# Kernel tuning notes

Hardware: AMD Instinct MI355X
Metric: run time of the kernel (lower is better)

Reference implementation:

```python
import jax, jax.numpy as jnp
import numpy as np
import math

S, HID = 2048, 2048
NH, Q_LORA, KV_LORA = 16, 1536, 512
NOPE, ROPE, VDIM = 128, 64, 128
HEAD = NOPE + ROPE  # 192
BLK = 128
EPS = 1e-6
MSCALE = 0.1 * 1.0 * math.log(40.0) + 1.0
SOFTMAX_SCALE = HEAD ** -0.5 * MSCALE * MSCALE


def _dequant(w, s, blk=BLK):
    # w: [out,in] stored quantized values, s: [ceil(out/blk), ceil(in/blk)] block scale_inv
    so = jnp.repeat(s, blk, axis=0)[: w.shape[0]]
    se = jnp.repeat(so, blk, axis=1)[:, : w.shape[1]]
    return w * se


def _mm_dq(x, w, s):
    # mm_w8a16_dq_forward: x @ dequant(w).T
    return x @ _dequant(w, s).T


def _rmsnorm(x, w, eps=EPS):
    var = jnp.mean(x * x, axis=-1, keepdims=True)
    return x * jax.lax.rsqrt(var + eps) * w


def _rotate_half(x):
    h = x.shape[-1] // 2
    return jnp.concatenate([-x[..., h:], x[..., :h]], axis=-1)


def setup_inputs() -> dict:
    key = jax.random.key(0)
    ks = jax.random.split(key, 16)
    d = {
        'hidden_states': jax.random.normal(ks[0], (S, HID), jnp.float32),
        'wq_a': jax.random.normal(ks[1], (Q_LORA, HID), jnp.float32),
        'sq_a': jax.random.uniform(ks[2], (12, 16), jnp.float32) * 0.02 + 0.005,
        'wq_b': jax.random.normal(ks[3], (NH * HEAD, Q_LORA), jnp.float32),
        'sq_b': jax.random.uniform(ks[4], (24, 12), jnp.float32) * 0.02 + 0.005,
        'wkv_a': jax.random.normal(ks[5], (KV_LORA + ROPE, HID), jnp.float32),
        'skv_a': jax.random.uniform(ks[6], (5, 16), jnp.float32) * 0.02 + 0.005,
        'wkv_b': jax.random.normal(ks[7], (NH * (NOPE + VDIM), KV_LORA), jnp.float32),
        'skv_b': jax.random.uniform(ks[8], (32, 4), jnp.float32) * 0.02 + 0.005,
        'wo': jax.random.normal(ks[9], (HID, NH * VDIM), jnp.float32),
        'so': jax.random.uniform(ks[10], (16, 16), jnp.float32) * 0.02 + 0.005,
        'q_ln_w': jnp.ones((Q_LORA,), jnp.float32),
        'kv_ln_w': jnp.ones((KV_LORA,), jnp.float32),
    }
    pos = jnp.arange(S, dtype=jnp.float32)[:, None]
    inv = 1.0 / (10000.0 ** (jnp.arange(0, ROPE, 2, dtype=jnp.float32) / ROPE))
    ang = pos * inv[None, :]
    ang = jnp.concatenate([ang, ang], axis=-1)  # [S, 64]
    d['cos'] = jnp.cos(ang)
    d['sin'] = jnp.sin(ang)
    return d


def reference(hidden_states, cos, sin, wq_a, sq_a, wq_b, sq_b, wkv_a, skv_a,
              wkv_b, skv_b, wo, so, q_ln_w, kv_ln_w):
    # Q low-rank path: q_a -> rmsnorm -> q_b
    lq = _mm_dq(hidden_states, wq_a, sq_a)                 # [S, q_lora]
    q = _mm_dq(_rmsnorm(lq, q_ln_w), wq_b, sq_b)           # [S, NH*HEAD]
    q = q.reshape(S, NH, HEAD)
    q_nope, q_pe = q[..., :NOPE], q[..., NOPE:]            # [S,NH,128], [S,NH,64]

    # KV low-rank + MQA rope path
    lkv = _mm_dq(hidden_states, wkv_a, skv_a)              # [S, kv_lora+rope]
    kv_nope = _rmsnorm(lkv[:, :KV_LORA], kv_ln_w)          # [S, kv_lora]
    k_pe = lkv[:, KV_LORA:]                                # [S, 64] (shared across heads)
    kvb = _mm_dq(kv_nope, wkv_b, skv_b).reshape(S, NH, NOPE + VDIM)
    k_nope, v = kvb[..., :NOPE], kvb[..., NOPE:]           # [S,NH,128] each

    # RoPE (rotate-half) on the pe parts
    q_pe = q_pe * cos[:, None, :] + _rotate_half(q_pe) * sin[:, None, :]
    k_pe = k_pe * cos + _rotate_half(k_pe) * sin           # [S, 64]

    # prefill MLA attention with causal mask
    scores = (jnp.einsum('shd,thd->hst', q_nope, k_nope)
              + jnp.einsum('shd,td->hst', q_pe, k_pe)) * SOFTMAX_SCALE
    causal = jnp.tril(jnp.ones((S, S), bool))
    scores = jnp.where(causal[None], scores, -jnp.inf)
    probs = jax.nn.softmax(scores, axis=-1)                # [NH,S,S]
    attn = jnp.einsum('hst,thd->shd', probs, v).reshape(S, NH * VDIM)

    return _mm_dq(attn, wo, so)                            # [S, HID]
```

## Files before the change

### kernel.cpp

```cpp
#include <hip/hip_runtime.h>
#include <hip/hip_bf16.h>

typedef unsigned short u16;
typedef unsigned int u32;
typedef __attribute__((ext_vector_type(8))) short bf16x8;
typedef __attribute__((ext_vector_type(4))) float f32x4;
typedef __attribute__((ext_vector_type(16))) float f32x16;
typedef __attribute__((ext_vector_type(4))) unsigned short u16x4;

#define S_LEN 2048
#define HIDDEN 2048
#define NHEAD 16
#define QLORA 1536
#define KVLORA 512
#define NOPE_D 128
#define ROPE_D 64
#define V_D 128
#define HEAD_D 192
#define NCOMB 2176
#define LOG2E 1.442695041f

__device__ __constant__ float SM_SCALE_C = (float)(0.07216878364870323 *
    ((0.1 * 3.6888794541139363 + 1.0) * (0.1 * 3.6888794541139363 + 1.0)));

__device__ inline u16 f2bf(float f) {
    __hip_bfloat16 h = __float2bfloat16(f);
    return *reinterpret_cast<u16*>(&h);
}
__device__ inline u32 pack2bf(float lo, float hi) {
    float2 v = make_float2(lo, hi);
    __hip_bfloat162 h2 = __float22bfloat162_rn(v);
    return *reinterpret_cast<u32*>(&h2);
}
__device__ inline float bf2f(u16 b) {
    union { unsigned int u; float f; } v; v.u = ((unsigned int)b) << 16;
    return v.f;
}
__device__ inline void gload_lds16(const u16* g, u16* l) {
    __builtin_amdgcn_global_load_lds(
        (const __attribute__((address_space(1))) void*)g,
        (__attribute__((address_space(3))) void*)l, 16, 0, 0);
}

__device__ __forceinline__ int xcd_swizzle(int orig, int nwg) {
    int qq = nwg >> 3, rr = nwg & 7, xcd = orig & 7, loc = orig >> 3;
    return (xcd < rr) ? (xcd * (qq + 1) + loc)
                      : (rr * (qq + 1) + (xcd - rr) * qq + loc);
}

__global__ __launch_bounds__(256)
void prep_weights(const float* __restrict__ hs,
                  const float* __restrict__ wq_a, const float* __restrict__ sq_a,
                  const float* __restrict__ wq_b, const float* __restrict__ sq_b,
                  const float* __restrict__ wkv_a, const float* __restrict__ skv_a,
                  const float* __restrict__ wkv_b, const float* __restrict__ skv_b,
                  const float* __restrict__ wo, const float* __restrict__ so,
                  u16* __restrict__ hs_bf, u16* __restrict__ wcomb,
                  u16* __restrict__ wqb_bf, u16* __restrict__ wkvb_bf,
                  u16* __restrict__ wo_bf) {
    int r = blockIdx.x * 4 + (threadIdx.x >> 6);
    const float* W; const float* Sc; u16* out; int n, K, sc_cols;
    if (r < 2048)       { W = hs;    Sc = 0;      out = hs_bf;   n = r;        K = 2048; sc_cols = 0; }
    else if (r < 3584)  { W = wq_a;  Sc = sq_a;   out = wcomb;   n = r - 2048; K = 2048; sc_cols = 16; }
    else if (r < 4160)  { W = wkv_a; Sc = skv_a;  out = wcomb + (size_t)QLORA * 2048; n = r - 3584; K = 2048; sc_cols = 16; }
    else if (r < 7232)  { W = wq_b;  Sc = sq_b;   out = wqb_bf;  n = r - 4160; K = 1536; sc_cols = 12; }
    else if (r < 11328) { W = wkv_b; Sc = skv_b;  out = wkvb_bf; n = r - 7232; K = 512;  sc_cols = 4; }
    else                { W = wo;    Sc = so;     out = wo_bf;   n = r - 11328; K = 2048; sc_cols = 16; }
    for (int k = (threadIdx.x & 63) * 8; k < K; k += 512) {
        float sc = Sc ? Sc[(n >> 7) * sc_cols + (k >> 7)] : 1.0f;
        f32x4 v0 = *(const f32x4*)(W + (size_t)n * K + k);
        f32x4 v1 = *(const f32x4*)(W + (size_t)n * K + k + 4);
        u32 w[4];
        w[0] = pack2bf(v0[0] * sc, v0[1] * sc);
        w[1] = pack2bf(v0[2] * sc, v0[3] * sc);
        w[2] = pack2bf(v1[0] * sc, v1[1] * sc);
        w[3] = pack2bf(v1[2] * sc, v1[3] * sc);
        *(__attribute__((ext_vector_type(4))) u32*)(out + (size_t)n * K + k) =
            *( __attribute__((ext_vector_type(4))) u32*)w;
    }
}

__device__ __forceinline__ void gemm_core(
    const u16* __restrict__ A, const u16* __restrict__ W, u16* __restrict__ C,
    int M, int N, int Ktot, int Ksub, int bm, int bn, int bz,
    u16 (*As)[128 * 64], u16 (*Ws)[128 * 64]) {
    const int tid = threadIdx.x;
    const int lane = tid & 63;
    const int wv = tid >> 6;
    const int wm = wv >> 1, wn = wv & 1;
    const int lr = lane & 15, lk = lane >> 4;
    const int srow = lane >> 3;
    const int schunk = lane & 7;

    f32x4 acc[4][4] = {};

    const int kbeg = bz * Ksub;
    const int nst = Ksub >> 6;

    auto stage = [&](int buf, int k0) {
        #pragma unroll
        for (int i = 0; i < 4; ++i) {
            int t = (wv * 4 + i) * 8 + srow;
            int cs = (schunk ^ (t & 7)) << 3;
            gload_lds16(A + (size_t)(bm + t) * Ktot + k0 + cs, &As[buf][(wv * 4 + i) * 512]);
            gload_lds16(W + (size_t)(bn + t) * Ktot + k0 + cs, &Ws[buf][(wv * 4 + i) * 512]);
        }
    };

    stage(0, kbeg);
    __syncthreads();
    int cur = 0;
    for (int t = 0; t < nst; ++t) {
        if (t + 1 < nst) stage(cur ^ 1, kbeg + (t + 1) * 64);
        #pragma unroll
        for (int kh = 0; kh < 2; ++kh) {
            bf16x8 af[4], bfr[4];
            #pragma unroll
            for (int mi = 0; mi < 4; ++mi) {
                int r = wm * 64 + mi * 16 + lr;
                af[mi] = *(const bf16x8*)&As[cur][r * 64 + (((kh * 4 + lk) ^ (lr & 7)) << 3)];
            }
            #pragma unroll
            for (int ni = 0; ni < 4; ++ni) {
                int r = wn * 64 + ni * 16 + lr;
                bfr[ni] = *(const bf16x8*)&Ws[cur][r * 64 + (((kh * 4 + lk) ^ (lr & 7)) << 3)];
            }
            __builtin_amdgcn_s_setprio(1);
            #pragma unroll
            for (int mi = 0; mi < 4; ++mi)
                #pragma unroll
                for (int ni = 0; ni < 4; ++ni)
                    acc[mi][ni] = __builtin_amdgcn_mfma_f32_16x16x32_bf16(af[mi], bfr[ni], acc[mi][ni], 0, 0, 0);
            __builtin_amdgcn_s_setprio(0);
        }
        __syncthreads();
        cur ^= 1;
    }

    u16* Pb = C + (size_t)bz * M * N;
    #pragma unroll
    for (int mi = 0; mi < 4; ++mi)
        #pragma unroll
        for (int ni = 0; ni < 4; ++ni)
            #pragma unroll
            for (int j = 0; j < 4; ++j) {
                int r = bm + wm * 64 + mi * 16 + lk * 4 + j;
                int c = bn + wn * 64 + ni * 16 + lr;
                if (c < N) Pb[(size_t)r * N + c] = f2bf(acc[mi][ni][j]);
            }
}

__global__ __launch_bounds__(256)
void gemm_bf16(const u16* __restrict__ A, const u16* __restrict__ W,
               u16* __restrict__ C, int M, int N, int Ktot, int Ksub) {
    __shared__ u16 As[2][128 * 64];
    __shared__ u16 Ws[2][128 * 64];
    const int gx = gridDim.x, gy = gridDim.y;
    const int nwg = gx * gy * gridDim.z;
    const int orig = blockIdx.x + gx * (blockIdx.y + gy * blockIdx.z);
    const int wg = xcd_swizzle(orig, nwg);
    const int bn = (wg % gx) * 128;
    const int bm = ((wg / gx) % gy) * 128;
    const int bz = wg / (gx * gy);
    gemm_core(A, W, C, M, N, Ktot, Ksub, bm, bn, bz, As, Ws);
}

__global__ __launch_bounds__(256)
void gemm_qh_kvb(const u16* __restrict__ lqn, const u16* __restrict__ wqb, u16* __restrict__ arena,
                 const u16* __restrict__ kvn, const u16* __restrict__ wkvb, u16* __restrict__ kvb) {
    __shared__ u16 As[2][128 * 64];
    __shared__ u16 Ws[2][128 * 64];
    const int NWG = 24 * 16 * 3 + 32 * 16;
    const int wg = xcd_swizzle(blockIdx.x, NWG);
    if (wg < 24 * 16 * 3) {
        const int bn = (wg % 24) * 128;
        const int bm = ((wg / 24) % 16) * 128;
        const int bz = wg / (24 * 16);
        gemm_core(lqn, wqb, arena, S_LEN, NHEAD * HEAD_D, QLORA, 512, bm, bn, bz, As, Ws);
    } else {
        const int w2 = wg - 24 * 16 * 3;
        const int bn = (w2 % 32) * 128;
        const int bm = (w2 / 32) * 128;
        gemm_core(kvn, wkvb, kvb, S_LEN, NHEAD * 256, KVLORA, 512, bm, bn, 0, As, Ws);
    }
}

__global__ __launch_bounds__(256)
void reduce_rms_comb(const u16* __restrict__ P,
                     const float* __restrict__ q_ln, const float* __restrict__ kv_ln,
                     u16* __restrict__ lqn, u16* __restrict__ kvn, u16* __restrict__ kpe) {
    __shared__ float vbuf[NCOMB];
    __shared__ float r2[2][4];
    const int row = blockIdx.x;
    const u16* p0 = P + (size_t)row * NCOMB;
    const size_t st = (size_t)S_LEN * NCOMB;
    float ssq = 0.f, ssk = 0.f;
    for (int c = threadIdx.x * 8; c < NCOMB; c += 2048) {
        bf16x8 a0 = *(const bf16x8*)(p0 + c);
        bf16x8 a1 = *(const bf16x8*)(p0 + st + c);
        bf16x8 a2 = *(const bf16x8*)(p0 + 2 * st + c);
        bf16x8 a3 = *(const bf16x8*)(p0 + 3 * st + c);
        float s = 0.f;
        #pragma unroll
        for (int j = 0; j < 8; ++j) {
            float v = bf2f((u16)a0[j]) + bf2f((u16)a1[j]) + bf2f((u16)a2[j]) + bf2f((u16)a3[j]);
            vbuf[c + j] = v;
            s += v * v;
        }
        if (c < QLORA) ssq += s;
        else if (c < QLORA + KVLORA) ssk += s;
    }
    #pragma unroll
    for (int off = 1; off < 64; off <<= 1) {
        ssq += __shfl_xor(ssq, off, 64);
        ssk += __shfl_xor(ssk, off, 64);
    }
    if ((threadIdx.x & 63) == 0) {
        r2[0][threadIdx.x >> 6] = ssq;
        r2[1][threadIdx.x >> 6] = ssk;
    }
    __syncthreads();
    float rsq = rsqrtf((r2[0][0] + r2[0][1] + r2[0][2] + r2[0][3]) / (float)QLORA + 1e-6f);
    float rsk = rsqrtf((r2[1][0] + r2[1][1] + r2[1][2] + r2[1][3]) / (float)KVLORA + 1e-6f);
    for (int c = threadIdx.x * 8; c < NCOMB; c += 2048) {
        bf16x8 o;
        if (c < QLORA) {
            #pragma unroll
            for (int j = 0; j < 8; ++j) o[j] = (short)f2bf(vbuf[c + j] * rsq * q_ln[c + j]);
            *(bf16x8*)(lqn + (size_t)row * QLORA + c) = o;
        } else if (c < QLORA + KVLORA) {
            int cc = c - QLORA;
            #pragma unroll
            for (int j = 0; j < 8; ++j) o[j] = (short)f2bf(vbuf[c + j] * rsk * kv_ln[cc + j]);
            *(bf16x8*)(kvn + (size_t)row * KVLORA + cc) = o;
        } else if (c < QLORA + KVLORA + ROPE_D) {
            int cc = c - QLORA - KVLORA;
            #pragma unroll
            for (int j = 0; j < 8; ++j) o[j] = (short)f2bf(vbuf[c + j]);
            *(bf16x8*)(kpe + (size_t)row * ROPE_D + cc) = o;
        }
    }
}

__global__ __launch_bounds__(256)
void prep_qkv_frag(const u16* __restrict__ P, const u16* __restrict__ kvb,
                   const u16* __restrict__ kpe, const float* __restrict__ cosb,
                   const float* __restrict__ sinb, u16* __restrict__ qfrag,
                   u16* __restrict__ kfrag, u16* __restrict__ vfrag) {
    __shared__ u16 Vs[32][136];
    const int sblk = blockIdx.x, h = blockIdx.y;
    if (blockIdx.z == 0) {
        const float sm = SM_SCALE_C;
        const size_t st = (size_t)S_LEN * (NHEAD * HEAD_D);
        #pragma unroll
        for (int c = 0; c < 3; ++c) {
            int idx = c * 256 + threadIdx.x;
            int kk = idx >> 6;
            int lane = idx & 63;
            int s = sblk * 32 + (lane & 31);
            int d0 = kk * 16 + (lane >> 5) * 8;
            const u16* p0 = P + (size_t)s * (NHEAD * HEAD_D) + h * HEAD_D;
            float x[8];
            {
                bf16x8 a0 = *(const bf16x8*)(p0 + d0);
                bf16x8 a1 = *(const bf16x8*)(p0 + st + d0);
                bf16x8 a2 = *(const bf16x8*)(p0 + 2 * st + d0);
                #pragma unroll
                for (int j = 0; j < 8; ++j)
                    x[j] = bf2f((u16)a0[j]) + bf2f((u16)a1[j]) + bf2f((u16)a2[j]);
            }
            bf16x8 o;
            if (d0 < NOPE_D) {
                #pragma unroll
                for (int j = 0; j < 8; ++j) o[j] = (short)f2bf(x[j] * sm);
            } else {
                int r0 = d0 - NOPE_D;
                int rp = (r0 + 32) & 63;
                float rv[8];
                bf16x8 b0 = *(const bf16x8*)(p0 + NOPE_D + rp);
                bf16x8 b1 = *(const bf16x8*)(p0 + st + NOPE_D + rp);
                bf16x8 b2 = *(const bf16x8*)(p0 + 2 * st + NOPE_D + rp);
                #pragma unroll
                for (int j = 0; j < 8; ++j)
                    rv[j] = bf2f((u16)b0[j]) + bf2f((u16)b1[j]) + bf2f((u16)b2[j]);
                float sign = (r0 < 32) ? -1.f : 1.f;
                #pragma unroll
                for (int j = 0; j < 8; ++j) {
                    float cs = cosb[s * ROPE_D + r0 + j];
                    float sn = sinb[s * ROPE_D + r0 + j];
                    o[j] = (short)f2bf((x[j] * cs + sign * rv[j] * sn) * sm);
                }
            }
            *(bf16x8*)(qfrag + (((size_t)h * 64 + sblk) * 12 + kk) * 512 + lane * 8) = o;
        }
    } else {
        #pragma unroll
        for (int it = 0; it < 2; ++it) {
            int idx = it * 256 + threadIdx.x;
            int r = idx >> 4;
            int c8 = (idx & 15) * 8;
            int s = sblk * 32 + r;
            *(bf16x8*)&Vs[r][c8] = *(const bf16x8*)(kvb + (size_t)s * (NHEAD * 256) + h * 256 + NOPE_D + c8);
        }
        #pragma unroll
        for (int c = 0; c < 3; ++c) {
            int idx = c * 256 + threadIdx.x;
            int kk = idx >> 6;
            int lane = idx & 63;
            int s = sblk * 32 + (lane & 31);
            int d0 = kk * 16 + (lane >> 5) * 8;
            bf16x8 o;
            if (d0 < NOPE_D) {
                o = *(const bf16x8*)(kvb + (size_t)s * (NHEAD * 256) + h * 256 + d0);
            } else {
                int r0 = d0 - NOPE_D;
                const u16* kp = kpe + (size_t)s * ROPE_D;
                bf16x8 x = *(const bf16x8*)(kp + r0);
                bf16x8 rv = *(const bf16x8*)(kp + ((r0 + 32) & 63));
                float sign = (r0 < 32) ? -1.f : 1.f;
                #pragma unroll
                for (int j = 0; j < 8; ++j) {
                    float cs = cosb[s * ROPE_D + r0 + j];
                    float sn = sinb[s * ROPE_D + r0 + j];
                    o[j] = (short)f2bf(bf2f((u16)x[j]) * cs + sign * bf2f((u16)rv[j]) * sn);
                }
            }
            *(bf16x8*)(kfrag + (((size_t)h * 64 + sblk) * 12 + kk) * 512 + lane * 8) = o;
        }
        __syncthreads();
        #pragma unroll
        for (int it = 0; it < 2; ++it) {
            int idx = it * 256 + threadIdx.x;
            int fi = idx >> 6;
            int lane = idx & 63;
            int bb = fi >> 1, h16 = fi & 1;
            int col = bb * 32 + (lane & 31);
            int row0 = h16 * 16 + (lane >> 5) * 8;
            bf16x8 o;
            #pragma unroll
            for (int j = 0; j < 8; ++j) o[j] = (short)Vs[row0 + j][col];
            *(bf16x8*)(vfrag + (((size_t)h * 64 + sblk) * 8 + fi) * 512 + lane * 8) = o;
        }
    }
}

__global__ void reduce_out(const u16* __restrict__ P, float* __restrict__ out, int n) {
    int i = (blockIdx.x * blockDim.x + threadIdx.x) * 8;
    if (i >= n) return;
    bf16x8 a0 = *(const bf16x8*)(P + i);
    bf16x8 a1 = *(const bf16x8*)(P + (size_t)n + i);
    bf16x8 a2 = *(const bf16x8*)(P + 2 * (size_t)n + i);
    bf16x8 a3 = *(const bf16x8*)(P + 3 * (size_t)n + i);
    f32x4 o0, o1;
    #pragma unroll
    for (int j = 0; j < 4; ++j) {
        o0[j] = bf2f((u16)a0[j]) + bf2f((u16)a1[j]) + bf2f((u16)a2[j]) + bf2f((u16)a3[j]);
        o1[j] = bf2f((u16)a0[j + 4]) + bf2f((u16)a1[j + 4]) + bf2f((u16)a2[j + 4]) + bf2f((u16)a3[j + 4]);
    }
    *(f32x4*)(out + i) = o0;
    *(f32x4*)(out + i + 4) = o1;
}

__global__ __launch_bounds__(256, 2)
void flash_attn4(const u16* __restrict__ qfrag, const u16* __restrict__ kfrag,
                 const u16* __restrict__ vfrag, u16* __restrict__ attn) {
    __shared__ float OB[3][128][32];
    __shared__ float MB[3][2][32];

    const int tid = threadIdx.x, lane = tid & 63, wq = tid >> 6;
    const int b = blockIdx.x;
    const int t = 63 - (b >> 4);
    const int h = ((b & 7) << 1) | ((b >> 3) & 1);
    const int q0 = t * 32;
    const int lq = lane & 31;
    const int hi = lane >> 5;

    const int n = t + 1;
    const int s_lo = (wq * n) >> 2;
    const int s_hi = ((wq + 1) * n) >> 2;

    bf16x8 qfr[12];
    {
        const u16* qb = qfrag + (((size_t)h * 64 + t) * 12) * 512 + lane * 8;
        #pragma unroll
        for (int kk = 0; kk < 12; ++kk) qfr[kk] = *(const bf16x8*)(qb + kk * 512);
    }

    const u16* kfb = kfrag + ((size_t)h * 64 * 12) * 512 + lane * 8;
    const u16* vfb = vfrag + ((size_t)h * 64 * 8) * 512 + lane * 8;

    f32x16 oa[4] = {};
    float mrun = -3.0e38f, lrun = 0.f;

    bf16x8 kcur[12], vcur[8];
    {
        int psub = (s_lo < s_hi) ? s_lo : 0;
        const u16* kp = kfb + (size_t)psub * 12 * 512;
        #pragma unroll
        for (int kk = 0; kk < 12; ++kk)
            kcur[kk] = *(const bf16x8*)(kp + kk * 512);
        const u16* vp = vfb + (size_t)psub * 8 * 512;
        #pragma unroll
        for (int fi = 0; fi < 8; ++fi)
            vcur[fi] = *(const bf16x8*)(vp + fi * 512);
    }

    for (int sub = s_lo; sub < s_hi; ++sub) {
        f32x16 s0 = {}, s1 = {};
        __builtin_amdgcn_s_setprio(1);
        #pragma unroll
        for (int kk = 0; kk < 12; kk += 2) {
            s0 = __builtin_amdgcn_mfma_f32_32x32x16_bf16(kcur[kk], qfr[kk], s0, 0, 0, 0);
            s1 = __builtin_amdgcn_mfma_f32_32x32x16_bf16(kcur[kk + 1], qfr[kk + 1], s1, 0, 0, 0);
        }
        __builtin_amdgcn_s_setprio(0);
        {
            int nsub = (sub + 1 < s_hi) ? sub + 1 : sub;
            const u16* kp = kfb + (size_t)nsub * 12 * 512;
            #pragma unroll
            for (int kk = 0; kk < 12; ++kk)
                kcur[kk] = *(const bf16x8*)(kp + kk * 512);
        }
        f32x16 sv = s0 + s1;
        if (sub == t) {
            #pragma unroll
            for (int r = 0; r < 16; ++r) {
                int krow = (r & 3) + 8 * (r >> 2) + 4 * hi;
                if (krow > lq) sv[r] = -3.0e38f;
            }
        }
        float tm = sv[0];
        #pragma unroll
        for (int r = 1; r < 16; ++r) tm = fmaxf(tm, sv[r]);
        tm = fmaxf(tm, __shfl_xor(tm, 32, 64));
        if (!__all(tm - mrun <= 8.f)) {
            float mn = fmaxf(mrun, tm);
            float scl = exp2f((mrun - mn) * LOG2E);
            mrun = mn;
            lrun *= scl;
            #pragma unroll
            for (int bb = 0; bb < 4; ++bb)
                #pragma unroll
                for (int r = 0; r < 16; ++r) oa[bb][r] *= scl;
        }
        float p[16];
        float psum = 0.f;
        #pragma unroll
        for (int r = 0; r < 16; ++r) {
            p[r] = exp2f((sv[r] - mrun) * LOG2E);
            psum += p[r];
        }
        psum += __shfl_xor(psum, 32, 64);
        lrun += psum;
        u32 pw[8], sw[8];
        #pragma unroll
        for (int i = 0; i < 8; ++i)
            pw[i] = pack2bf(p[2 * i], p[2 * i + 1]);
        #pragma unroll
        for (int i = 0; i < 8; ++i)
            sw[i] = (u32)__shfl_xor((int)pw[i], 32, 64);
        union { u32 w[4]; bf16x8 v; } bf0, bf1;
        bf0.w[0] = hi ? sw[2] : pw[0];
        bf0.w[1] = hi ? sw[3] : pw[1];
        bf0.w[2] = hi ? pw[2] : sw[0];
        bf0.w[3] = hi ? pw[3] : sw[1];
        bf1.w[0] = hi ? sw[6] : pw[4];
        bf1.w[1] = hi ? sw[7] : pw[5];
        bf1.w[2] = hi ? pw[6] : sw[4];
        bf1.w[3] = hi ? pw[7] : sw[5];
        __builtin_amdgcn_s_setprio(1);
        #pragma unroll
        for (int bb = 0; bb < 4; ++bb) {
            oa[bb] = __builtin_amdgcn_mfma_f32_32x32x16_bf16(vcur[bb * 2],     bf0.v, oa[bb], 0, 0, 0);
            oa[bb] = __builtin_amdgcn_mfma_f32_32x32x16_bf16(vcur[bb * 2 + 1], bf1.v, oa[bb], 0, 0, 0);
        }
        __builtin_amdgcn_s_setprio(0);
        {
            int nsub = (sub + 1 < s_hi) ? sub + 1 : sub;
            const u16* vp = vfb + (size_t)nsub * 8 * 512;
            #pragma unroll
            for (int fi = 0; fi < 8; ++fi)
                vcur[fi] = *(const bf16x8*)(vp + fi * 512);
        }
    }

    if (wq) {
        #pragma unroll
        for (int bb = 0; bb < 4; ++bb)
            #pragma unroll
            for (int r = 0; r < 16; ++r) {
                int dv = bb * 32 + (r & 3) + 8 * (r >> 2) + 4 * hi;
                OB[wq - 1][dv][lq] = oa[bb][r];
            }
        if (lane < 32) {
            MB[wq - 1][0][lane] = mrun;
            MB[wq - 1][1][lane] = lrun;
        }
    }
    __syncthreads();
    if (!wq) {
        float m1 = MB[0][0][lq], l1 = MB[0][1][lq];
        float m2 = MB[1][0][lq], l2 = MB[1][1][lq];
        float m3 = MB[2][0][lq], l3 = MB[2][1][lq];
        float M = fmaxf(fmaxf(mrun, m1), fmaxf(m2, m3));
        float e0 = exp2f((mrun - M) * LOG2E);
        float e1 = exp2f((m1 - M) * LOG2E);
        float e2 = exp2f((m2 - M) * LOG2E);
        float e3 = exp2f((m3 - M) * LOG2E);
        float L = lrun * e0 + l1 * e1 + l2 * e2 + l3 * e3;
        float inv = 1.0f / L;
        u16* ob = attn + (size_t)(q0 + lq) * (NHEAD * V_D) + h * V_D;
        #pragma unroll
        for (int bb = 0; bb < 4; ++bb)
            #pragma unroll
            for (int rq = 0; rq < 4; ++rq) {
                u16x4 pk;
                #pragma unroll
                for (int rb = 0; rb < 4; ++rb) {
                    int r = rq * 4 + rb;
                    int dv = bb * 32 + rb + 8 * rq + 4 * hi;
                    float o = (oa[bb][r] * e0 + OB[0][dv][lq] * e1 +
                               OB[1][dv][lq] * e2 + OB[2][dv][lq] * e3) * inv;
                    pk[rb] = f2bf(o);
                }
                *(u16x4*)(ob + bb * 32 + 8 * rq + 4 * hi) = pk;
            }
    }
}

extern "C" void kernel_launch(void* const* d_in, const int* in_sizes, int n_in,
                              void* d_out, int out_size, void* d_ws, size_t ws_size,
                              hipStream_t stream) {
    const float* hs    = (const float*)d_in[0];
    const float* wq_a  = (const float*)d_in[1];
    const float* sq_a  = (const float*)d_in[2];
    const float* wq_b  = (const float*)d_in[3];
    const float* sq_b  = (const float*)d_in[4];
    const float* wkv_a = (const float*)d_in[5];
    const float* skv_a = (const float*)d_in[6];
    const float* wkv_b = (const float*)d_in[7];
    const float* skv_b = (const float*)d_in[8];
    const float* wo    = (const float*)d_in[9];
    const float* so    = (const float*)d_in[10];
    const float* q_ln  = (const float*)d_in[11];
    const float* kv_ln = (const float*)d_in[12];
    const float* cosb  = (const float*)d_in[13];
    const float* sinb  = (const float*)d_in[14];
    float* out = (float*)d_out;

    char* ws = (char*)d_ws;
    size_t off = 0;
    auto alloc = [&](size_t bytes) -> void* {
        void* p = ws + off; off += (bytes + 255) & ~(size_t)255; return p;
    };
    u16* hs_bf  = (u16*)alloc((size_t)S_LEN * HIDDEN * 2);
    u16* lqn    = (u16*)alloc((size_t)S_LEN * QLORA * 2);
    u16* kvn    = (u16*)alloc((size_t)S_LEN * KVLORA * 2);
    u16* kpe    = (u16*)alloc((size_t)S_LEN * ROPE_D * 2);
    u16* kvb    = (u16*)alloc((size_t)S_LEN * NHEAD * 256 * 2);
    u16* attn   = (u16*)alloc((size_t)S_LEN * NHEAD * V_D * 2);
    u16* qfrag  = (u16*)alloc((size_t)NHEAD * 64 * 12 * 512 * 2);
    u16* kfrag  = (u16*)alloc((size_t)NHEAD * 64 * 12 * 512 * 2);
    u16* vfrag  = (u16*)alloc((size_t)NHEAD * 64 * 8 * 512 * 2);
    u16* wcomb  = (u16*)alloc((size_t)NCOMB * HIDDEN * 2);
    u16* wqb_bf  = (u16*)alloc((size_t)(NHEAD * HEAD_D) * QLORA * 2);
    u16* wkvb_bf = (u16*)alloc((size_t)(NHEAD * 256) * KVLORA * 2);
    u16* wo_bf   = (u16*)alloc((size_t)HIDDEN * (NHEAD * V_D) * 2);
    u16* arena  = (u16*)alloc((size_t)3 * S_LEN * (NHEAD * HEAD_D) * 2);

    prep_weights<<<3344, 256, 0, stream>>>(
        hs, wq_a, sq_a, wq_b, sq_b, wkv_a, skv_a, wkv_b, skv_b, wo, so,
        hs_bf, wcomb, wqb_bf, wkvb_bf, wo_bf);

    gemm_bf16<<<dim3(NCOMB / 128, S_LEN / 128, 4), 256, 0, stream>>>(hs_bf, wcomb, arena,
        S_LEN, NCOMB, HIDDEN, HIDDEN / 4);
    reduce_rms_comb<<<S_LEN, 256, 0, stream>>>(arena, q_ln, kv_ln, lqn, kvn, kpe);

    gemm_qh_kvb<<<24 * 16 * 3 + 32 * 16, 256, 0, stream>>>(lqn, wqb_bf, arena, kvn, wkvb_bf, kvb);

    prep_qkv_frag<<<dim3(64, NHEAD, 2), 256, 0, stream>>>(arena, kvb, kpe, cosb, sinb,
        qfrag, kfrag, vfrag);

    flash_attn4<<<1024, 256, 0, stream>>>(qfrag, kfrag, vfrag, attn);

    gemm_bf16<<<dim3(16, 16, 4), 256, 0, stream>>>(attn, wo_bf, arena,
        S_LEN, HIDDEN, NHEAD * V_D, (NHEAD * V_D) / 4);
    reduce_out<<<S_LEN * HIDDEN / 8 / 256, 256, 0, stream>>>(arena, out, S_LEN * HIDDEN);
}
```

Measured before the change: 197.4 us.

## Halve GEMM K-tile to 32 and reorganize LDS layout into 16-row groups

Shrinks the GEMM k-step from 64 to 32, which halves the LDS footprint per buffer (from 32KB to 16KB total per operand pair). It reorganizes staging so each 16-row group is loaded contiguously with an XOR-swizzled row order, letting fragments be read with one address per lane. The smaller LDS use may allow more resident workgroups for occupancy. In exchange it doubles the number of barriers and loop iterations per K, with fewer MFMAs to hide each load.

```diff
diff --git a/kernel.cpp b/kernel.cpp
--- a/kernel.cpp
+++ b/kernel.cpp
@@ -83,56 +83,52 @@
 __device__ __forceinline__ void gemm_core(
     const u16* __restrict__ A, const u16* __restrict__ W, u16* __restrict__ C,
     int M, int N, int Ktot, int Ksub, int bm, int bn, int bz,
-    u16 (*As)[128 * 64], u16 (*Ws)[128 * 64]) {
+    u16 (*As)[4096], u16 (*Ws)[4096]) {
     const int tid = threadIdx.x;
     const int lane = tid & 63;
     const int wv = tid >> 6;
     const int wm = wv >> 1, wn = wv & 1;
     const int lr = lane & 15, lk = lane >> 4;
-    const int srow = lane >> 3;
-    const int schunk = lane & 7;
+
+    const int sc_ = lane >> 4;
+    const int sr_ = ((lane >> 3) & 1) * 8 + ((lane & 7) ^ sc_);
+    const int sk_ = sc_ * 8;
 
     f32x4 acc[4][4] = {};
 
     const int kbeg = bz * Ksub;
-    const int nst = Ksub >> 6;
+    const int nst = Ksub >> 5;
 
     auto stage = [&](int buf, int k0) {
         #pragma unroll
-        for (int i = 0; i < 4; ++i) {
-            int t = (wv * 4 + i) * 8 + srow;
-            int cs = (schunk ^ (t & 7)) << 3;
-            gload_lds16(A + (size_t)(bm + t) * Ktot + k0 + cs, &As[buf][(wv * 4 + i) * 512]);
-            gload_lds16(W + (size_t)(bn + t) * Ktot + k0 + cs, &Ws[buf][(wv * 4 + i) * 512]);
+        for (int p = 0; p < 2; ++p) {
+            int g = p * 4 + wv;
+            gload_lds16(A + (size_t)(bm + g * 16 + sr_) * Ktot + k0 + sk_, &As[buf][g * 512]);
+            gload_lds16(W + (size_t)(bn + g * 16 + sr_) * Ktot + k0 + sk_, &Ws[buf][g * 512]);
         }
     };
+
+    const int fA = lk * 16 + (lr & 8) + ((lr & 7) ^ lk);
 
     stage(0, kbeg);
     __syncthreads();
     int cur = 0;
     for (int t = 0; t < nst; ++t) {
-        if (t + 1 < nst) stage(cur ^ 1, kbeg + (t + 1) * 64);
-        #pragma unroll
-        for (int kh = 0; kh < 2; ++kh) {
-            bf16x8 af[4], bfr[4];
-            #pragma unroll
-            for (int mi = 0; mi < 4; ++mi) {
-                int r = wm * 64 + mi * 16 + lr;
-                af[mi] = *(const bf16x8*)&As[cur][r * 64 + (((kh * 4 + lk) ^ (lr & 7)) << 3)];
-            }
-            #pragma unroll
-            for (int ni = 0; ni < 4; ++ni) {
-                int r = wn * 64 + ni * 16 + lr;
-                bfr[ni] = *(const bf16x8*)&Ws[cur][r * 64 + (((kh * 4 + lk) ^ (lr & 7)) << 3)];
-            }
-            __builtin_amdgcn_s_setprio(1);
-            #pragma unroll
-            for (int mi = 0; mi < 4; ++mi)
-                #pragma unroll
-                for (int ni = 0; ni < 4; ++ni)
-                    acc[mi][ni] = __builtin_amdgcn_mfma_f32_16x16x32_bf16(af[mi], bfr[ni], acc[mi][ni], 0, 0, 0);
-            __builtin_amdgcn_s_setprio(0);
-        }
+        if (t + 1 < nst) stage(cur ^ 1, kbeg + (t + 1) * 32);
+        bf16x8 af[4], bfr[4];
+        #pragma unroll
+        for (int mi = 0; mi < 4; ++mi)
+            af[mi] = *(const bf16x8*)&As[cur][(wm * 4 + mi) * 512 + fA * 8];
+        #pragma unroll
+        for (int ni = 0; ni < 4; ++ni)
+            bfr[ni] = *(const bf16x8*)&Ws[cur][(wn * 4 + ni) * 512 + fA * 8];
+        __builtin_amdgcn_s_setprio(1);
+        #pragma unroll
+        for (int mi = 0; mi < 4; ++mi)
+            #pragma unroll
+            for (int ni = 0; ni < 4; ++ni)
+                acc[mi][ni] = __builtin_amdgcn_mfma_f32_16x16x32_bf16(af[mi], bfr[ni], acc[mi][ni], 0, 0, 0);
+        __builtin_amdgcn_s_setprio(0);
         __syncthreads();
         cur ^= 1;
     }
@@ -153,8 +149,8 @@
 __global__ __launch_bounds__(256)
 void gemm_bf16(const u16* __restrict__ A, const u16* __restrict__ W,
                u16* __restrict__ C, int M, int N, int Ktot, int Ksub) {
-    __shared__ u16 As[2][128 * 64];
-    __shared__ u16 Ws[2][128 * 64];
+    __shared__ u16 As[2][4096];
+    __shared__ u16 Ws[2][4096];
     const int gx = gridDim.x, gy = gridDim.y;
     const int nwg = gx * gy * gridDim.z;
     const int orig = blockIdx.x + gx * (blockIdx.y + gy * blockIdx.z);
@@ -168,8 +164,8 @@
 __global__ __launch_bounds__(256)
 void gemm_qh_kvb(const u16* __restrict__ lqn, const u16* __restrict__ wqb, u16* __restrict__ arena,
                  const u16* __restrict__ kvn, const u16* __restrict__ wkvb, u16* __restrict__ kvb) {
-    __shared__ u16 As[2][128 * 64];
-    __shared__ u16 Ws[2][128 * 64];
+    __shared__ u16 As[2][4096];
+    __shared__ u16 Ws[2][4096];
     const int NWG = 24 * 16 * 3 + 32 * 16;
     const int wg = xcd_swizzle(blockIdx.x, NWG);
     if (wg < 24 * 16 * 3) {
```

New measurement: 244.4 us. +23.8%, slower.
